# Kernel optimization log

Measured on AMD Instinct MI355X. Metric: run time of the kernel, lower is better.

## Reference

```python
import jax, jax.numpy as jnp
import numpy as np

H = 16
D_MODEL = 1024
D_K = D_MODEL // H
B, S = 8, 1024


def setup_inputs() -> dict:
    key = jax.random.key(0)
    ks = jax.random.split(key, 11)
    scale = 1.0 / np.sqrt(D_MODEL)
    inp = {
        "query": jax.random.normal(ks[0], (B, S, D_MODEL), jnp.float32),
        "key_": jax.random.normal(ks[1], (B, S, D_MODEL), jnp.float32),
        "value": jax.random.normal(ks[2], (B, S, D_MODEL), jnp.float32),
        "w_q": jax.random.normal(ks[3], (D_MODEL, D_MODEL), jnp.float32) * scale,
        "b_q": jnp.zeros((D_MODEL,), jnp.float32),
        "w_k": jax.random.normal(ks[4], (D_MODEL, D_MODEL), jnp.float32) * scale,
        "b_k": jnp.zeros((D_MODEL,), jnp.float32),
        "w_v": jax.random.normal(ks[5], (D_MODEL, D_MODEL), jnp.float32) * scale,
        "b_v": jnp.zeros((D_MODEL,), jnp.float32),
        "w_o": jax.random.normal(ks[6], (D_MODEL, D_MODEL), jnp.float32) * scale,
        "b_o": jnp.zeros((D_MODEL,), jnp.float32),
    }
    return inp


def reference(query, key_, value, w_q, b_q, w_k, b_k, w_v, b_v, w_o, b_o):
    # Linear projections (torch Linear: x @ W.T + b), then split heads: [B,S,D] -> [B,H,S,d_k]
    def proj(x, w, b):
        y = jnp.einsum("bsd,ed->bse", x, w) + b
        return y.reshape(B, S, H, D_K).transpose(0, 2, 1, 3)

    q = proj(query, w_q, b_q)
    k = proj(key_, w_k, b_k)
    v = proj(value, w_v, b_v)

    # Scaled dot-product attention (mask=None, dropout p=0 -> identity)
    scores = jnp.einsum("bhqd,bhkd->bhqk", q, k) / jnp.sqrt(jnp.float32(D_K))
    attn = jax.nn.softmax(scores, axis=-1)
    ctx = jnp.einsum("bhqk,bhkd->bhqd", attn, v)  # [B,H,S,d_k]

    # Merge heads and final output projection
    ctx = ctx.transpose(0, 2, 1, 3).reshape(B, S, D_MODEL)
    return jnp.einsum("bsd,ed->bse", ctx, w_o) + b_o
```

## Files before the change

### kernel.cpp

```cpp
#include <hip/hip_runtime.h>
#include <hip/hip_bf16.h>

#define NH 16
#define DK 64
#define BB 8
#define SS 1024
#define DM 1024
#define MTOT (BB * SS)

typedef float f4v __attribute__((ext_vector_type(4)));
typedef float f16v __attribute__((ext_vector_type(16)));
typedef short s16v8 __attribute__((ext_vector_type(8)));
typedef unsigned short u16v4 __attribute__((ext_vector_type(4)));
typedef unsigned short u16v8 __attribute__((ext_vector_type(8)));

#define EXP2F(x) __builtin_amdgcn_exp2f(x)

__device__ __forceinline__ unsigned short f2bf(float x) {
    unsigned int u = __float_as_uint(x);
    u += 0x7FFFu + ((u >> 16) & 1u);
    return (unsigned short)(u >> 16);
}

__device__ __forceinline__ unsigned int packbf2(float lo, float hi) {
    return ((unsigned int)f2bf(hi) << 16) | f2bf(lo);
}

__device__ __forceinline__ void gload16(const void* g, void* l) {
    __builtin_amdgcn_global_load_lds(
        (const __attribute__((address_space(1))) void*)g,
        (__attribute__((address_space(3))) void*)l, 16, 0, 0);
}

struct Src7 { const float* p[7]; };

__global__ __launch_bounds__(256) void cvt_all(Src7 sp, unsigned short* __restrict__ dst) {
    const size_t e = ((size_t)blockIdx.x * 256 + threadIdx.x) * 8;
    const int unit = (int)(e >> 20);
    int t; size_t base;
    if (unit < 8)       { t = 0; base = 0; }
    else if (unit < 16) { t = 1; base = (size_t)8 << 20; }
    else if (unit < 24) { t = 2; base = (size_t)16 << 20; }
    else                { t = 3 + (unit - 24); base = (size_t)unit << 20; }
    const float* s = sp.p[t] + (e - base);
    f4v a = *(const f4v*)s;
    f4v b = *(const f4v*)(s + 4);
    u16v8 o;
    o[0] = f2bf(a[0]); o[1] = f2bf(a[1]); o[2] = f2bf(a[2]); o[3] = f2bf(a[3]);
    o[4] = f2bf(b[0]); o[5] = f2bf(b[1]); o[6] = f2bf(b[2]); o[7] = f2bf(b[3]);
    *(u16v8*)(dst + e) = o;
}

struct QkvArgs {
    const unsigned short* X[3];
    const unsigned short* W[3];
    const float* bias[3];
    unsigned short* Y[3];
};

__global__ __launch_bounds__(256) void gemm_qkv(QkvArgs a) {
    __shared__ unsigned short As[128 * 32];
    __shared__ unsigned short Bs[128 * 32];
    const int z = blockIdx.z;
    const unsigned short* X = a.X[z];
    const unsigned short* W = a.W[z];
    const float* bias = a.bias[z];
    unsigned short* Y = a.Y[z];

    const int tid = threadIdx.x;
    const int wv = tid >> 6, l = tid & 63;
    const int lq = l & 15, g = l >> 4;
    const int wr = wv >> 1, wc = wv & 1;
    const int m0 = blockIdx.y * 128, n0 = blockIdx.x * 128;

    f4v acc[4][4];
#pragma unroll
    for (int i = 0; i < 4; ++i)
#pragma unroll
        for (int j = 0; j < 4; ++j) acc[i][j] = (f4v){0.f, 0.f, 0.f, 0.f};

    for (int kt = 0; kt < DM / 32; ++kt) {
        const int k0 = kt * 32;
        __syncthreads();
#pragma unroll
        for (int p = 0; p < 2; ++p) {
            const int u = p * 256 + tid;
            const int row = u >> 2, kc = u & 3;
            gload16(X + (size_t)(m0 + row) * DM + k0 + kc * 8, As + (size_t)u * 8);
            gload16(W + (size_t)(n0 + row) * DM + k0 + kc * 8, Bs + (size_t)u * 8);
        }
        __syncthreads();

        s16v8 av[4], bv[4];
#pragma unroll
        for (int i = 0; i < 4; ++i)
            av[i] = *(const s16v8*)(As + (wr * 64 + i * 16 + lq) * 32 + g * 8);
#pragma unroll
        for (int j = 0; j < 4; ++j)
            bv[j] = *(const s16v8*)(Bs + (wc * 64 + j * 16 + lq) * 32 + g * 8);
#pragma unroll
        for (int i = 0; i < 4; ++i)
#pragma unroll
            for (int j = 0; j < 4; ++j)
                acc[i][j] = __builtin_amdgcn_mfma_f32_16x16x32_bf16(av[i], bv[j], acc[i][j], 0, 0, 0);
    }

#pragma unroll
    for (int j = 0; j < 4; ++j) {
        const int col = n0 + wc * 64 + j * 16 + lq;
        const float bvl = bias[col];
#pragma unroll
        for (int i = 0; i < 4; ++i) {
            const int row0 = m0 + wr * 64 + i * 16 + g * 4;
            if (z < 2) {
#pragma unroll
                for (int r = 0; r < 4; ++r) {
                    const int row = row0 + r;
                    const int b_ = row >> 10, s_ = row & (SS - 1);
                    const int h_ = col >> 6, d_ = col & (DK - 1);
                    Y[((size_t)(b_ * NH + h_) * SS + s_) * DK + d_] = f2bf(acc[i][j][r] + bvl);
                }
            } else {
                const int b_ = row0 >> 10, s0_ = row0 & (SS - 1);
                const int h_ = col >> 6, d_ = col & (DK - 1);
                u16v4 o;
#pragma unroll
                for (int r = 0; r < 4; ++r) o[r] = f2bf(acc[i][j][r] + bvl);
                *(u16v4*)&Y[((size_t)(b_ * NH + h_) * DK + d_) * SS + s0_] = o;
            }
        }
    }
}

__global__ __launch_bounds__(256) void gemm_out(const unsigned short* __restrict__ X,
                                                const unsigned short* __restrict__ W,
                                                const float* __restrict__ bias,
                                                float* __restrict__ Y) {
    __shared__ unsigned short As[128 * 32];
    __shared__ unsigned short Bs[128 * 32];
    const int tid = threadIdx.x;
    const int wv = tid >> 6, l = tid & 63;
    const int lq = l & 15, g = l >> 4;
    const int wr = wv >> 1, wc = wv & 1;
    const int m0 = blockIdx.y * 128, n0 = blockIdx.x * 128;

    f4v acc[4][4];
#pragma unroll
    for (int i = 0; i < 4; ++i)
#pragma unroll
        for (int j = 0; j < 4; ++j) acc[i][j] = (f4v){0.f, 0.f, 0.f, 0.f};

    for (int kt = 0; kt < DM / 32; ++kt) {
        const int k0 = kt * 32;
        __syncthreads();
#pragma unroll
        for (int p = 0; p < 2; ++p) {
            const int u = p * 256 + tid;
            const int row = u >> 2, kc = u & 3;
            gload16(X + (size_t)(m0 + row) * DM + k0 + kc * 8, As + (size_t)u * 8);
            gload16(W + (size_t)(n0 + row) * DM + k0 + kc * 8, Bs + (size_t)u * 8);
        }
        __syncthreads();

        s16v8 av[4], bv[4];
#pragma unroll
        for (int i = 0; i < 4; ++i)
            av[i] = *(const s16v8*)(As + (wr * 64 + i * 16 + lq) * 32 + g * 8);
#pragma unroll
        for (int j = 0; j < 4; ++j)
            bv[j] = *(const s16v8*)(Bs + (wc * 64 + j * 16 + lq) * 32 + g * 8);
#pragma unroll
        for (int i = 0; i < 4; ++i)
#pragma unroll
            for (int j = 0; j < 4; ++j)
                acc[i][j] = __builtin_amdgcn_mfma_f32_16x16x32_bf16(av[i], bv[j], acc[i][j], 0, 0, 0);
    }

#pragma unroll
    for (int j = 0; j < 4; ++j) {
        const int col = n0 + wc * 64 + j * 16 + lq;
        const float bvl = bias[col];
#pragma unroll
        for (int i = 0; i < 4; ++i) {
#pragma unroll
            for (int r = 0; r < 4; ++r) {
                const int row = m0 + wr * 64 + i * 16 + g * 4 + r;
                Y[(size_t)row * DM + col] = acc[i][j][r] + bvl;
            }
        }
    }
}

__global__ __launch_bounds__(256) void attn_mfma32(const unsigned short* __restrict__ Qp,
                                                   const unsigned short* __restrict__ Kp,
                                                   const unsigned short* __restrict__ Vt,
                                                   unsigned short* __restrict__ ctx) {
    const int tid = threadIdx.x;
    const int wv = tid >> 6;
    const int l = tid & 63;
    const int l31 = l & 31, hi = l >> 5;
    const int bh = blockIdx.x;
    const int q = blockIdx.y * 128 + wv * 32 + l31;
    const float C = 0.18033688011112042f;

    const unsigned short* Qrow = Qp + ((size_t)bh * SS + q) * DK + hi * 8;
    s16v8 qf[4];
#pragma unroll
    for (int kd = 0; kd < 4; ++kd) qf[kd] = *(const s16v8*)(Qrow + kd * 16);

    const unsigned short* Kb = Kp + (size_t)bh * SS * DK + hi * 8;
    const unsigned short* Vb = Vt + (size_t)bh * DK * SS + hi * 8;

    f16v O0, O1;
#pragma unroll
    for (int r = 0; r < 16; ++r) { O0[r] = 0.f; O1[r] = 0.f; }
    float me = -1e30f;
    float lr = 0.f;

    for (int t = 0; t < SS / 64; ++t) {
        s16v8 kf[2][4];
#pragma unroll
        for (int ks = 0; ks < 2; ++ks)
#pragma unroll
            for (int kd = 0; kd < 4; ++kd)
                kf[ks][kd] = *(const s16v8*)(Kb + (size_t)(t * 64 + ks * 32 + l31) * DK + kd * 16);
        s16v8 vf[2][4];
#pragma unroll
        for (int db = 0; db < 2; ++db)
#pragma unroll
            for (int ksg = 0; ksg < 4; ++ksg)
                vf[db][ksg] = *(const s16v8*)(Vb + (size_t)(db * 32 + l31) * SS + t * 64 + ksg * 16);

        f16v s0, s1;
#pragma unroll
        for (int r = 0; r < 16; ++r) { s0[r] = 0.f; s1[r] = 0.f; }
#pragma unroll
        for (int kd = 0; kd < 4; ++kd) {
            s0 = __builtin_amdgcn_mfma_f32_32x32x16_bf16(kf[0][kd], qf[kd], s0, 0, 0, 0);
            s1 = __builtin_amdgcn_mfma_f32_32x32x16_bf16(kf[1][kd], qf[kd], s1, 0, 0, 0);
        }

        float mx = s0[0];
#pragma unroll
        for (int r = 1; r < 16; ++r) mx = fmaxf(mx, s0[r]);
#pragma unroll
        for (int r = 0; r < 16; ++r) mx = fmaxf(mx, s1[r]);
        mx = fmaxf(mx, __shfl_xor(mx, 32));
        const float mxl = mx * C;

        const bool need = !__all(mxl - me <= 8.0f);
        float corr = 1.0f;
        if (need) {
            const float mnew = fmaxf(me, mxl);
            corr = EXP2F(me - mnew);
            me = mnew;
        }

        float rs = 0.f;
#pragma unroll
        for (int r = 0; r < 16; ++r) { s0[r] = EXP2F(__fmaf_rn(s0[r], C, -me)); rs += s0[r]; }
#pragma unroll
        for (int r = 0; r < 16; ++r) { s1[r] = EXP2F(__fmaf_rn(s1[r], C, -me)); rs += s1[r]; }
        rs += __shfl_xor(rs, 32);
        if (need) {
            lr = lr * corr + rs;
#pragma unroll
            for (int r = 0; r < 16; ++r) { O0[r] *= corr; O1[r] *= corr; }
        } else {
            lr += rs;
        }

        s16v8 pb[2][2];
#pragma unroll
        for (int ks = 0; ks < 2; ++ks) {
            unsigned int u[8], su[8];
#pragma unroll
            for (int i = 0; i < 8; ++i) {
                const float plo = (ks == 0) ? s0[2 * i] : s1[2 * i];
                const float phi = (ks == 0) ? s0[2 * i + 1] : s1[2 * i + 1];
                u[i] = packbf2(plo, phi);
            }
#pragma unroll
            for (int i = 0; i < 8; ++i) su[i] = (unsigned int)__shfl_xor((int)u[i], 32);
#pragma unroll
            for (int kk = 0; kk < 2; ++kk) {
                const int base = 4 * kk + 2 * hi;
                union { unsigned int w[4]; s16v8 s; } f;
                f.w[0] = hi ? su[base] : u[base];
                f.w[1] = hi ? su[base + 1] : u[base + 1];
                f.w[2] = hi ? u[base] : su[base];
                f.w[3] = hi ? u[base + 1] : su[base + 1];
                pb[ks][kk] = f.s;
            }
        }

#pragma unroll
        for (int ksg = 0; ksg < 4; ++ksg) {
            O0 = __builtin_amdgcn_mfma_f32_32x32x16_bf16(vf[0][ksg], pb[ksg >> 1][ksg & 1], O0, 0, 0, 0);
            O1 = __builtin_amdgcn_mfma_f32_32x32x16_bf16(vf[1][ksg], pb[ksg >> 1][ksg & 1], O1, 0, 0, 0);
        }
    }

    const float inv = 1.0f / lr;
    const int b_ = bh >> 4, h_ = bh & 15;
    unsigned short* crow = ctx + ((size_t)b_ * SS + q) * DM + h_ * DK;
#pragma unroll
    for (int g2 = 0; g2 < 4; ++g2) {
        u16v4 o0, o1;
#pragma unroll
        for (int r2 = 0; r2 < 4; ++r2) {
            o0[r2] = f2bf(O0[4 * g2 + r2] * inv);
            o1[r2] = f2bf(O1[4 * g2 + r2] * inv);
        }
        *(u16v4*)(crow + 8 * g2 + 4 * hi) = o0;
        *(u16v4*)(crow + 32 + 8 * g2 + 4 * hi) = o1;
    }
}

extern "C" void kernel_launch(void* const* d_in, const int* in_sizes, int n_in,
                              void* d_out, int out_size, void* d_ws, size_t ws_size,
                              hipStream_t stream) {
    const float* query = (const float*)d_in[0];
    const float* key_  = (const float*)d_in[1];
    const float* value = (const float*)d_in[2];
    const float* w_q = (const float*)d_in[3];
    const float* b_q = (const float*)d_in[4];
    const float* w_k = (const float*)d_in[5];
    const float* b_k = (const float*)d_in[6];
    const float* w_v = (const float*)d_in[7];
    const float* b_v = (const float*)d_in[8];
    const float* w_o = (const float*)d_in[9];
    const float* b_o = (const float*)d_in[10];

    unsigned short* ws = (unsigned short*)d_ws;
    const size_t NX = (size_t)MTOT * DM;
    const size_t NW = (size_t)DM * DM;
    unsigned short* xq  = ws;
    unsigned short* xk  = xq + NX;
    unsigned short* xv  = xk + NX;
    unsigned short* wqb = xv + NX;
    unsigned short* wkb = wqb + NW;
    unsigned short* wvb = wkb + NW;
    unsigned short* wob = wvb + NW;
    unsigned short* Qp  = wob + NW;
    unsigned short* Kp  = Qp + NX;
    unsigned short* VpT = Kp + NX;
    unsigned short* ctx = xq;

    Src7 sp;
    sp.p[0] = query; sp.p[1] = key_; sp.p[2] = value;
    sp.p[3] = w_q; sp.p[4] = w_k; sp.p[5] = w_v; sp.p[6] = w_o;
    cvt_all<<<14336, 256, 0, stream>>>(sp, ws);

    QkvArgs qa;
    qa.X[0] = xq;  qa.X[1] = xk;  qa.X[2] = xv;
    qa.W[0] = wqb; qa.W[1] = wkb; qa.W[2] = wvb;
    qa.bias[0] = b_q; qa.bias[1] = b_k; qa.bias[2] = b_v;
    qa.Y[0] = Qp; qa.Y[1] = Kp; qa.Y[2] = VpT;
    gemm_qkv<<<dim3(DM / 128, MTOT / 128, 3), 256, 0, stream>>>(qa);

    attn_mfma32<<<dim3(BB * NH, SS / 128), 256, 0, stream>>>(Qp, Kp, VpT, ctx);

    gemm_out<<<dim3(DM / 128, MTOT / 128), 256, 0, stream>>>(ctx, wob, b_o, (float*)d_out);
}
```

Before: 441.0 us.

## Prefetch K tiles in attention, stage output through LDS, swap GEMM grid order

The attention loop now double-buffers K fragments, loading the next tile's K registers while computing the current one, and unrolls by two to alternate buffers. The attention epilogue writes normalized output to a swizzled LDS buffer, then emits 16-byte coalesced stores to ctx instead of scattered 8-byte stores. Launch bounds request two blocks per SM. Both GEMMs swap grid axes so consecutive blocks walk the M dimension, which changes which tiles share L2. The K prefetch raises register pressure, which may conflict with the occupancy hint.

```diff
diff --git a/kernel.cpp b/kernel.cpp
--- a/kernel.cpp
+++ b/kernel.cpp
@@ -71,7 +71,7 @@
     const int wv = tid >> 6, l = tid & 63;
     const int lq = l & 15, g = l >> 4;
     const int wr = wv >> 1, wc = wv & 1;
-    const int m0 = blockIdx.y * 128, n0 = blockIdx.x * 128;
+    const int m0 = blockIdx.x * 128, n0 = blockIdx.y * 128;
 
     f4v acc[4][4];
 #pragma unroll
@@ -142,7 +142,7 @@
     const int wv = tid >> 6, l = tid & 63;
     const int lq = l & 15, g = l >> 4;
     const int wr = wv >> 1, wc = wv & 1;
-    const int m0 = blockIdx.y * 128, n0 = blockIdx.x * 128;
+    const int m0 = blockIdx.x * 128, n0 = blockIdx.y * 128;
 
     f4v acc[4][4];
 #pragma unroll
@@ -191,25 +191,118 @@
     }
 }
 
-__global__ __launch_bounds__(256) void attn_mfma32(const unsigned short* __restrict__ Qp,
-                                                   const unsigned short* __restrict__ Kp,
-                                                   const unsigned short* __restrict__ Vt,
-                                                   unsigned short* __restrict__ ctx) {
+__device__ __forceinline__ void attn_iter(int t, int tn,
+                                          const unsigned short* __restrict__ Kb,
+                                          const unsigned short* __restrict__ Vb,
+                                          int l31, int hi,
+                                          const s16v8 (&qf)[4],
+                                          s16v8 (&ku)[2][4],
+                                          s16v8 (&kl)[2][4],
+                                          f16v& O0, f16v& O1, float& me, float& lr) {
+    const float C = 0.18033688011112042f;
+
+    s16v8 vf[2][4];
+#pragma unroll
+    for (int db = 0; db < 2; ++db)
+#pragma unroll
+        for (int ksg = 0; ksg < 4; ++ksg)
+            vf[db][ksg] = *(const s16v8*)(Vb + (size_t)(db * 32 + l31) * SS + t * 64 + ksg * 16 + hi * 8);
+#pragma unroll
+    for (int ks = 0; ks < 2; ++ks)
+#pragma unroll
+        for (int kd = 0; kd < 4; ++kd)
+            kl[ks][kd] = *(const s16v8*)(Kb + (size_t)(tn * 64 + ks * 32 + l31) * DK + kd * 16 + hi * 8);
+
+    f16v s0, s1;
+#pragma unroll
+    for (int r = 0; r < 16; ++r) { s0[r] = 0.f; s1[r] = 0.f; }
+#pragma unroll
+    for (int kd = 0; kd < 4; ++kd) {
+        s0 = __builtin_amdgcn_mfma_f32_32x32x16_bf16(ku[0][kd], qf[kd], s0, 0, 0, 0);
+        s1 = __builtin_amdgcn_mfma_f32_32x32x16_bf16(ku[1][kd], qf[kd], s1, 0, 0, 0);
+    }
+
+    float mx = s0[0];
+#pragma unroll
+    for (int r = 1; r < 16; ++r) mx = fmaxf(mx, s0[r]);
+#pragma unroll
+    for (int r = 0; r < 16; ++r) mx = fmaxf(mx, s1[r]);
+    mx = fmaxf(mx, __shfl_xor(mx, 32));
+    const float mxl = mx * C;
+
+    const bool need = !__all(mxl - me <= 8.0f);
+    float corr = 1.0f;
+    if (need) {
+        const float mnew = fmaxf(me, mxl);
+        corr = EXP2F(me - mnew);
+        me = mnew;
+    }
+
+    float rs = 0.f;
+#pragma unroll
+    for (int r = 0; r < 16; ++r) { s0[r] = EXP2F(__fmaf_rn(s0[r], C, -me)); rs += s0[r]; }
+#pragma unroll
+    for (int r = 0; r < 16; ++r) { s1[r] = EXP2F(__fmaf_rn(s1[r], C, -me)); rs += s1[r]; }
+    rs += __shfl_xor(rs, 32);
+    if (need) {
+        lr = lr * corr + rs;
+#pragma unroll
+        for (int r = 0; r < 16; ++r) { O0[r] *= corr; O1[r] *= corr; }
+    } else {
+        lr += rs;
+    }
+
+    s16v8 pb[2][2];
+#pragma unroll
+    for (int ks = 0; ks < 2; ++ks) {
+        unsigned int u[8], su[8];
+#pragma unroll
+        for (int i = 0; i < 8; ++i) {
+            const float plo = (ks == 0) ? s0[2 * i] : s1[2 * i];
+            const float phi = (ks == 0) ? s0[2 * i + 1] : s1[2 * i + 1];
+            u[i] = packbf2(plo, phi);
+        }
+#pragma unroll
+        for (int i = 0; i < 8; ++i) su[i] = (unsigned int)__shfl_xor((int)u[i], 32);
+#pragma unroll
+        for (int kk = 0; kk < 2; ++kk) {
+            const int base = 4 * kk + 2 * hi;
+            union { unsigned int w[4]; s16v8 s; } f;
+            f.w[0] = hi ? su[base] : u[base];
+            f.w[1] = hi ? su[base + 1] : u[base + 1];
+            f.w[2] = hi ? u[base] : su[base];
+            f.w[3] = hi ? u[base + 1] : su[base + 1];
+            pb[ks][kk] = f.s;
+        }
+    }
+
+#pragma unroll
+    for (int ksg = 0; ksg < 4; ++ksg) {
+        O0 = __builtin_amdgcn_mfma_f32_32x32x16_bf16(vf[0][ksg], pb[ksg >> 1][ksg & 1], O0, 0, 0, 0);
+        O1 = __builtin_amdgcn_mfma_f32_32x32x16_bf16(vf[1][ksg], pb[ksg >> 1][ksg & 1], O1, 0, 0, 0);
+    }
+}
+
+__global__ __launch_bounds__(256, 2) void attn_mfma32(const unsigned short* __restrict__ Qp,
+                                                      const unsigned short* __restrict__ Kp,
+                                                      const unsigned short* __restrict__ Vt,
+                                                      unsigned short* __restrict__ ctx) {
+    __shared__ unsigned short Ob[4][2048];
     const int tid = threadIdx.x;
     const int wv = tid >> 6;
     const int l = tid & 63;
     const int l31 = l & 31, hi = l >> 5;
     const int bh = blockIdx.x;
-    const int q = blockIdx.y * 128 + wv * 32 + l31;
-    const float C = 0.18033688011112042f;
+    const int qblk = blockIdx.y;
+    const int q = qblk * 128 + wv * 32 + l31;
 
     const unsigned short* Qrow = Qp + ((size_t)bh * SS + q) * DK + hi * 8;
     s16v8 qf[4];
 #pragma unroll
     for (int kd = 0; kd < 4; ++kd) qf[kd] = *(const s16v8*)(Qrow + kd * 16);
 
-    const unsigned short* Kb = Kp + (size_t)bh * SS * DK + hi * 8;
-    const unsigned short* Vb = Vt + (size_t)bh * DK * SS + hi * 8;
+    const unsigned short* Kb = Kp + (size_t)bh * SS * DK;
+    const unsigned short* Vb = Vt + (size_t)bh * DK * SS;
 
     f16v O0, O1;
 #pragma unroll
@@ -217,103 +310,44 @@
     float me = -1e30f;
     float lr = 0.f;
 
-    for (int t = 0; t < SS / 64; ++t) {
-        s16v8 kf[2][4];
-#pragma unroll
-        for (int ks = 0; ks < 2; ++ks)
-#pragma unroll
-            for (int kd = 0; kd < 4; ++kd)
-                kf[ks][kd] = *(const s16v8*)(Kb + (size_t)(t * 64 + ks * 32 + l31) * DK + kd * 16);
-        s16v8 vf[2][4];
-#pragma unroll
-        for (int db = 0; db < 2; ++db)
-#pragma unroll
-            for (int ksg = 0; ksg < 4; ++ksg)
-                vf[db][ksg] = *(const s16v8*)(Vb + (size_t)(db * 32 + l31) * SS + t * 64 + ksg * 16);
-
-        f16v s0, s1;
-#pragma unroll
-        for (int r = 0; r < 16; ++r) { s0[r] = 0.f; s1[r] = 0.f; }
-#pragma unroll
-        for (int kd = 0; kd < 4; ++kd) {
-            s0 = __builtin_amdgcn_mfma_f32_32x32x16_bf16(kf[0][kd], qf[kd], s0, 0, 0, 0);
-            s1 = __builtin_amdgcn_mfma_f32_32x32x16_bf16(kf[1][kd], qf[kd], s1, 0, 0, 0);
-        }
-
-        float mx = s0[0];
-#pragma unroll
-        for (int r = 1; r < 16; ++r) mx = fmaxf(mx, s0[r]);
-#pragma unroll
-        for (int r = 0; r < 16; ++r) mx = fmaxf(mx, s1[r]);
-        mx = fmaxf(mx, __shfl_xor(mx, 32));
-        const float mxl = mx * C;
-
-        const bool need = !__all(mxl - me <= 8.0f);
-        float corr = 1.0f;
-        if (need) {
-            const float mnew = fmaxf(me, mxl);
-            corr = EXP2F(me - mnew);
-            me = mnew;
-        }
-
-        float rs = 0.f;
-#pragma unroll
-        for (int r = 0; r < 16; ++r) { s0[r] = EXP2F(__fmaf_rn(s0[r], C, -me)); rs += s0[r]; }
-#pragma unroll
-        for (int r = 0; r < 16; ++r) { s1[r] = EXP2F(__fmaf_rn(s1[r], C, -me)); rs += s1[r]; }
-        rs += __shfl_xor(rs, 32);
-        if (need) {
-            lr = lr * corr + rs;
-#pragma unroll
-            for (int r = 0; r < 16; ++r) { O0[r] *= corr; O1[r] *= corr; }
-        } else {
-            lr += rs;
-        }
-
-        s16v8 pb[2][2];
-#pragma unroll
-        for (int ks = 0; ks < 2; ++ks) {
-            unsigned int u[8], su[8];
-#pragma unroll
-            for (int i = 0; i < 8; ++i) {
-                const float plo = (ks == 0) ? s0[2 * i] : s1[2 * i];
-                const float phi = (ks == 0) ? s0[2 * i + 1] : s1[2 * i + 1];
-                u[i] = packbf2(plo, phi);
-            }
-#pragma unroll
-            for (int i = 0; i < 8; ++i) su[i] = (unsigned int)__shfl_xor((int)u[i], 32);
-#pragma unroll
-            for (int kk = 0; kk < 2; ++kk) {
-                const int base = 4 * kk + 2 * hi;
-                union { unsigned int w[4]; s16v8 s; } f;
-                f.w[0] = hi ? su[base] : u[base];
-                f.w[1] = hi ? su[base + 1] : u[base + 1];
-                f.w[2] = hi ? u[base] : su[base];
-                f.w[3] = hi ? u[base + 1] : su[base + 1];
-                pb[ks][kk] = f.s;
-            }
-        }
-
-#pragma unroll
-        for (int ksg = 0; ksg < 4; ++ksg) {
-            O0 = __builtin_amdgcn_mfma_f32_32x32x16_bf16(vf[0][ksg], pb[ksg >> 1][ksg & 1], O0, 0, 0, 0);
-            O1 = __builtin_amdgcn_mfma_f32_32x32x16_bf16(vf[1][ksg], pb[ksg >> 1][ksg & 1], O1, 0, 0, 0);
-        }
+    s16v8 kA[2][4], kB[2][4];
+#pragma unroll
+    for (int ks = 0; ks < 2; ++ks)
+#pragma unroll
+        for (int kd = 0; kd < 4; ++kd)
+            kA[ks][kd] = *(const s16v8*)(Kb + (size_t)(ks * 32 + l31) * DK + kd * 16 + hi * 8);
+
+    for (int tt = 0; tt < 8; ++tt) {
+        const int t0 = 2 * tt, t1 = 2 * tt + 1;
+        attn_iter(t0, t1, Kb, Vb, l31, hi, qf, kA, kB, O0, O1, me, lr);
+        attn_iter(t1, (t1 + 1 < 16) ? t1 + 1 : 15, Kb, Vb, l31, hi, qf, kB, kA, O0, O1, me, lr);
     }
 
     const float inv = 1.0f / lr;
+    unsigned short* mybuf = Ob[wv];
+#pragma unroll
+    for (int db = 0; db < 2; ++db) {
+        const f16v Ocur = db ? O1 : O0;
+#pragma unroll
+        for (int g2 = 0; g2 < 4; ++g2) {
+            uint2 w;
+            w.x = packbf2(Ocur[4 * g2 + 0] * inv, Ocur[4 * g2 + 1] * inv);
+            w.y = packbf2(Ocur[4 * g2 + 2] * inv, Ocur[4 * g2 + 3] * inv);
+            const int off = db * 64 + g2 * 16 + hi * 8;
+            *(uint2*)((char*)mybuf + l31 * 128 + (off ^ ((l31 & 7) << 4))) = w;
+        }
+    }
+    __syncthreads();
+
+    const int r = l >> 1, h2 = l & 1;
+    const int qrow = qblk * 128 + wv * 32 + r;
     const int b_ = bh >> 4, h_ = bh & 15;
-    unsigned short* crow = ctx + ((size_t)b_ * SS + q) * DM + h_ * DK;
-#pragma unroll
-    for (int g2 = 0; g2 < 4; ++g2) {
-        u16v4 o0, o1;
-#pragma unroll
-        for (int r2 = 0; r2 < 4; ++r2) {
-            o0[r2] = f2bf(O0[4 * g2 + r2] * inv);
-            o1[r2] = f2bf(O1[4 * g2 + r2] * inv);
-        }
-        *(u16v4*)(crow + 8 * g2 + 4 * hi) = o0;
-        *(u16v4*)(crow + 32 + 8 * g2 + 4 * hi) = o1;
+    unsigned short* crow = ctx + ((size_t)b_ * SS + qrow) * DM + h_ * DK + h2 * 32;
+#pragma unroll
+    for (int j = 0; j < 4; ++j) {
+        const int off = (h2 * 64 + j * 16) ^ ((r & 7) << 4);
+        u16v8 v = *(const u16v8*)((const char*)mybuf + r * 128 + off);
+        *(u16v8*)(crow + j * 8) = v;
     }
 }
 
@@ -357,9 +391,9 @@
     qa.W[0] = wqb; qa.W[1] = wkb; qa.W[2] = wvb;
     qa.bias[0] = b_q; qa.bias[1] = b_k; qa.bias[2] = b_v;
     qa.Y[0] = Qp; qa.Y[1] = Kp; qa.Y[2] = VpT;
-    gemm_qkv<<<dim3(DM / 128, MTOT / 128, 3), 256, 0, stream>>>(qa);
+    gemm_qkv<<<dim3(MTOT / 128, DM / 128, 3), 256, 0, stream>>>(qa);
 
     attn_mfma32<<<dim3(BB * NH, SS / 128), 256, 0, stream>>>(Qp, Kp, VpT, ctx);
 
-    gemm_out<<<dim3(DM / 128, MTOT / 128), 256, 0, stream>>>(ctx, wob, b_o, (float*)d_out);
-}
+    gemm_out<<<dim3(MTOT / 128, DM / 128), 256, 0, stream>>>(ctx, wob, b_o, (float*)d_out);
+}
```

Result: faster. 423.8 us (-3.9%).
